# Kernel optimization log

Hardware: AMD Instinct MI355X
Metric: run time of the kernel (lower is better)

## Reference

```python
import jax, jax.numpy as jnp
import numpy as np
import math

T, P, L, C, H, NPTS = 243, 17, 4, 128, 8, 4
DH = C // H


def _ln(x, g, b):
    m = jnp.mean(x, axis=-1, keepdims=True)
    v = jnp.mean((x - m) ** 2, axis=-1, keepdims=True)
    return (x - m) * jax.lax.rsqrt(v + 1e-5) * g + b


def _bilinear(v, grid):
    # v: [B, D, Hh, Ww]; grid: [B, Q, Pt, 2] in [-1,1], (x->W, y->H),
    # align_corners=False, zero padding (matches F.grid_sample in MSDeformAttn core)
    B, D, Hh, Ww = v.shape
    x = (grid[..., 0] + 1.0) * (Ww * 0.5) - 0.5
    y = (grid[..., 1] + 1.0) * (Hh * 0.5) - 0.5
    x0 = jnp.floor(x)
    y0 = jnp.floor(y)
    x0i = x0.astype(jnp.int32)
    y0i = y0.astype(jnp.int32)
    x1i = x0i + 1
    y1i = y0i + 1
    wx1 = x - x0
    wx0 = 1.0 - wx1
    wy1 = y - y0
    wy0 = 1.0 - wy1
    vf = v.reshape(B, D, Hh * Ww)
    Q, Pt = x.shape[1], x.shape[2]

    def gather(yi, xi):
        valid = ((yi >= 0) & (yi < Hh) & (xi >= 0) & (xi < Ww)).astype(v.dtype)
        idx = jnp.clip(yi, 0, Hh - 1) * Ww + jnp.clip(xi, 0, Ww - 1)
        g = jnp.take_along_axis(vf, idx.reshape(B, 1, Q * Pt), axis=2).reshape(B, D, Q, Pt)
        return g * valid[:, None]

    return (gather(y0i, x0i) * (wy0 * wx0)[:, None]
            + gather(y0i, x1i) * (wy0 * wx1)[:, None]
            + gather(y1i, x0i) * (wy1 * wx0)[:, None]
            + gather(y1i, x1i) * (wy1 * wx1)[:, None])  # [B, D, Q, Pt]


def _forward(x, ref_points, pe_buf, learn_pos, w_off, b_off, w_attn, b_attn,
             w_val, b_val, w_out, b_out, in_w, in_b, out_w, out_b,
             fc1_w, fc1_b, fc2_w, fc2_b, g1, be1, g2, be2, g3, be3):
    b, t, p, l, c = x.shape  # l = n_levels + 1
    Lq = t * p * L
    x0 = x[..., :1, :]
    xs = x[..., 1:, :].reshape(b, Lq, c)
    # --- subforward_self: norm_1 -> PE(query) -> MSDeformAttn ---
    xn = _ln(xs, g1, be1)
    q = (xn.reshape(b, t, p, L, c) + pe_buf + learn_pos).reshape(b, Lq, c)
    off = (q @ w_off.T + b_off).reshape(b, Lq, H, L, NPTS, 2)
    aw = jax.nn.softmax((q @ w_attn.T + b_attn).reshape(b, Lq, H, L * NPTS), axis=-1)
    aw = aw.reshape(b, Lq, H, L, NPTS)
    ref = jnp.broadcast_to(ref_points[:, :, :, None, :], (b, t, p, L, 2)).reshape(b, Lq, 2)
    normalizer = jnp.array([p, t], dtype=x.dtype)  # (W, H) per level
    loc = ref[:, :, None, None, None, :] + off / normalizer  # [b,Lq,H,L,Pt,2]
    grids = 2.0 * loc - 1.0
    val = (xn @ w_val.T + b_val).reshape(b, t, p, L, H, DH)
    v_maps = val.transpose(3, 0, 4, 5, 1, 2).reshape(L, b * H, DH, t, p)
    g = grids.transpose(3, 0, 2, 1, 4, 5).reshape(L, b * H, Lq, NPTS, 2)
    sampled = jax.vmap(_bilinear)(v_maps, g)  # [L, b*H, DH, Lq, Pt]
    aw_t = aw.transpose(3, 0, 2, 1, 4).reshape(L, b * H, 1, Lq, NPTS)
    o = jnp.sum(sampled * aw_t, axis=(0, 4))  # [b*H, DH, Lq]
    o = o.reshape(b, H, DH, Lq).transpose(0, 3, 1, 2).reshape(b, Lq, c)
    xs = (o @ w_out.T + b_out) + xs
    # --- concat level-0 back, cross (self) MHA over (p*l) tokens per frame ---
    xcat = jnp.concatenate([x0, xs.reshape(b, t, p, L, c)], axis=3).reshape(b * t, p * l, c)
    xn2 = _ln(xcat, g2, be2)
    qkv = xn2 @ in_w.T + in_b
    qh, kh, vh = jnp.split(qkv, 3, axis=-1)
    S = p * l
    qh = qh.reshape(b * t, S, H, DH)
    kh = kh.reshape(b * t, S, H, DH)
    vh = vh.reshape(b * t, S, H, DH)
    att = jax.nn.softmax(jnp.einsum('bqhd,bkhd->bhqk', qh, kh) / math.sqrt(DH), axis=-1)
    ca = jnp.einsum('bhqk,bkhd->bqhd', att, vh).reshape(b * t, S, c) @ out_w.T + out_b
    xcat = ca + xcat
    xr = xcat.reshape(b, t, p, l, c)
    # --- MLP block ---
    h = _ln(xr, g3, be3)
    h = jax.nn.gelu(h @ fc1_w.T + fc1_b, approximate=False) @ fc2_w.T + fc2_b
    return h + xr


def setup_inputs() -> dict:
    key = jax.random.key(0)
    ks = jax.random.split(key, 20)
    B = 2
    s = 0.02
    x = jax.random.normal(ks[0], (B, T, P, L + 1, C), jnp.float32)
    ref_points = jax.random.uniform(ks[1], (B, T, P, 2), dtype=jnp.float32)
    # sinusoidal PE buffer
    pos = np.arange(T, dtype=np.float32)[:, None]
    div = np.exp(np.arange(0, C, 2, dtype=np.float32) * (-math.log(10000.0) / C))
    ang = pos * div  # [T, C//2]
    pe = np.zeros((1, T, P, L, C), np.float32)
    pe[..., 0::2] = np.sin(ang)[None, :, None, None, :]
    pe[..., 1::2] = np.cos(ang)[None, :, None, None, :]
    rn = lambda k, shp: s * jax.random.normal(k, shp, jnp.float32)
    return {
        'x': x, 'ref_points': ref_points,
        'pe_buf': jnp.asarray(pe),
        'learn_pos': rn(ks[2], (1, T, P, L, C)),
        'w_off': rn(ks[3], (H * L * NPTS * 2, C)), 'b_off': rn(ks[4], (H * L * NPTS * 2,)),
        'w_attn': rn(ks[5], (H * L * NPTS, C)), 'b_attn': rn(ks[6], (H * L * NPTS,)),
        'w_val': rn(ks[7], (C, C)), 'b_val': rn(ks[8], (C,)),
        'w_out': rn(ks[9], (C, C)), 'b_out': rn(ks[10], (C,)),
        'in_w': rn(ks[11], (3 * C, C)), 'in_b': rn(ks[12], (3 * C,)),
        'out_w': rn(ks[13], (C, C)), 'out_b': rn(ks[14], (C,)),
        'fc1_w': rn(ks[15], (4 * C, C)), 'fc1_b': rn(ks[16], (4 * C,)),
        'fc2_w': rn(ks[17], (C, 4 * C)), 'fc2_b': rn(ks[18], (C,)),
        'g1': jnp.ones((C,), jnp.float32), 'be1': jnp.zeros((C,), jnp.float32),
        'g2': jnp.ones((C,), jnp.float32), 'be2': jnp.zeros((C,), jnp.float32),
        'g3': jnp.ones((C,), jnp.float32), 'be3': jnp.zeros((C,), jnp.float32),
    }


def reference(x, ref_points, pe_buf, learn_pos, w_off, b_off, w_attn, b_attn,
              w_val, b_val, w_out, b_out, in_w, in_b, out_w, out_b,
              fc1_w, fc1_b, fc2_w, fc2_b, g1, be1, g2, be2, g3, be3):
    return _forward(x, ref_points, pe_buf, learn_pos, w_off, b_off, w_attn, b_attn,
                    w_val, b_val, w_out, b_out, in_w, in_b, out_w, out_b,
                    fc1_w, fc1_b, fc2_w, fc2_b, g1, be1, g2, be2, g3, be3)
```

## Files before the change

### kernel.cpp

```cpp
#include <hip/hip_runtime.h>
#include <math.h>

#define T_ 243
#define P_ 17
#define L_ 4
#define C_ 128
#define H_ 8
#define NPTS_ 4
#define DH_ 16
#define B_ 2
#define LQ (T_*P_*L_)
#define NT1 (B_*LQ)
#define LL (L_+1)
#define S_ (P_*LL)
#define NT2 (B_*T_*P_*LL)

typedef __attribute__((ext_vector_type(8))) short short8v;
typedef __attribute__((ext_vector_type(4))) short short4v;
typedef __attribute__((ext_vector_type(4))) float float4v;

__device__ __forceinline__ unsigned short f2bf(float f){
  union { float f; unsigned u; } un; un.f = f;
  unsigned r = un.u + 0x7FFF + ((un.u >> 16) & 1);
  return (unsigned short)(r >> 16);
}
__device__ __forceinline__ float bf2f(unsigned short u){
  union { unsigned u; float f; } un; un.u = ((unsigned)u) << 16; return un.f;
}
__device__ __forceinline__ void dma16(const unsigned short* g, unsigned short* l){
  __builtin_amdgcn_global_load_lds(
      (const __attribute__((address_space(1))) void*)g,
      (__attribute__((address_space(3))) void*)l, 16, 0, 0);
}

__global__ void k_wcvt(const float* __restrict__ w0, const float* __restrict__ w1,
                       const float* __restrict__ w2, const float* __restrict__ w3,
                       const float* __restrict__ w4, const float* __restrict__ w5,
                       const float* __restrict__ w6, const float* __restrict__ w7,
                       unsigned short* __restrict__ dst){
  int i = blockIdx.x*256 + threadIdx.x;
  if (i >= 278528) return;
  float v;
  if      (i < 32768)  v = w0[i];
  else if (i < 49152)  v = w1[i-32768];
  else if (i < 65536)  v = w2[i-49152];
  else if (i < 81920)  v = w3[i-65536];
  else if (i < 131072) v = w4[i-81920];
  else if (i < 147456) v = w5[i-131072];
  else if (i < 212992) v = w6[i-147456];
  else                 v = w7[i-212992];
  dst[i] = f2bf(v);
}

__global__ __launch_bounds__(256) void k_ln1_q(
    const float* __restrict__ x, const float* __restrict__ pe,
    const float* __restrict__ lpos, const float* __restrict__ g1,
    const float* __restrict__ be1, unsigned short* __restrict__ xn,
    unsigned short* __restrict__ q) {
  int w = threadIdx.x >> 6; int lane = threadIdx.x & 63;
  int i = blockIdx.x*4 + w;
  int c = lane*2;
  int b = i / LQ; int r = i % LQ;
  int t = r / (P_*L_); int rp = r % (P_*L_);
  int p = rp / L_; int lv = rp % L_;
  const float* xrow = x + (((size_t)(b*T_+t)*P_ + p)*LL + 1 + lv)*C_;
  float2 v = *(const float2*)(xrow + c);
  float s1 = v.x + v.y, s2 = v.x*v.x + v.y*v.y;
  #pragma unroll
  for (int d=1; d<64; d<<=1){ s1 += __shfl_xor(s1,d); s2 += __shfl_xor(s2,d); }
  float mean = s1*(1.0f/C_);
  float var  = s2*(1.0f/C_) - mean*mean;
  float inv = rsqrtf(var + 1e-5f);
  float2 gg = *(const float2*)(g1 + c);
  float2 bb = *(const float2*)(be1 + c);
  float xn0 = (v.x - mean)*inv*gg.x + bb.x;
  float xn1 = (v.y - mean)*inv*gg.y + bb.y;
  size_t oi = (size_t)i*C_ + c;
  *(unsigned*)(xn + oi) = (unsigned)f2bf(xn0) | ((unsigned)f2bf(xn1) << 16);
  size_t pidx = (((size_t)t*P_ + p)*L_ + lv)*C_ + c;
  float2 pv = *(const float2*)(pe + pidx);
  float2 lp = *(const float2*)(lpos + pidx);
  *(unsigned*)(q + oi) = (unsigned)f2bf(xn0 + pv.x + lp.x) | ((unsigned)f2bf(xn1 + pv.y + lp.y) << 16);
}

__global__ __launch_bounds__(256) void k_ln(
    const float* __restrict__ in, const float* __restrict__ g,
    const float* __restrict__ be, unsigned short* __restrict__ out, int M){
  int w = threadIdx.x >> 6; int lane = threadIdx.x & 63;
  int i = blockIdx.x*4 + w;
  if (i >= M) return;
  int c = lane*2;
  float2 v = *(const float2*)(in + (size_t)i*C_ + c);
  float s1 = v.x + v.y, s2 = v.x*v.x + v.y*v.y;
  #pragma unroll
  for (int d=1; d<64; d<<=1){ s1 += __shfl_xor(s1,d); s2 += __shfl_xor(s2,d); }
  float mean = s1*(1.0f/C_);
  float var  = s2*(1.0f/C_) - mean*mean;
  float inv = rsqrtf(var + 1e-5f);
  float2 gg = *(const float2*)(g + c);
  float2 bb = *(const float2*)(be + c);
  float o0 = (v.x - mean)*inv*gg.x + bb.x;
  float o1 = (v.y - mean)*inv*gg.y + bb.y;
  *(unsigned*)(out + (size_t)i*C_ + c) = (unsigned)f2bf(o0) | ((unsigned)f2bf(o1) << 16);
}

template<int K, int N, int EPI>
__global__ __launch_bounds__(256) void k_mm(
    const unsigned short* __restrict__ A, const unsigned short* __restrict__ Bw,
    const float* __restrict__ bias, const float* __restrict__ res,
    float* __restrict__ outF, unsigned short* __restrict__ outB,
    const float* __restrict__ xres, int M)
{
  constexpr int NST = K / 128;
  __shared__ unsigned short As[64*128];
  __shared__ unsigned short Bs[128*128];
  int tid = threadIdx.x;
  int lane = tid & 63;
  int w = tid >> 6;
  int lr = lane & 15, kg = lane >> 4;
  int m0 = blockIdx.x * 64;
  int n0 = blockIdx.y * 128;
  int lrow = lane >> 4;
  int lch  = lane & 15;
  float4v acc[8] = {};
  for (int st = 0; st < NST; ++st){
    int kk = st*128;
    if (st) __syncthreads();
    #pragma unroll
    for (int j = 0; j < 4; ++j){
      int rb = w*16 + j*4;
      int srcch = lch ^ ((rb + lrow) & 7);
      dma16(A + (size_t)(m0 + rb + lrow)*K + kk + srcch*8, As + rb*128);
    }
    #pragma unroll
    for (int j = 0; j < 8; ++j){
      int rb = w*32 + j*4;
      int srcch = lch ^ ((rb + lrow) & 7);
      dma16(Bw + (size_t)(n0 + rb + lrow)*K + kk + srcch*8, Bs + rb*128);
    }
    __syncthreads();
    #pragma unroll
    for (int ks = 0; ks < 4; ++ks){
      int cn = ks*4 + kg;
      int arow = w*16 + lr;
      short8v af = *(const short8v*)(As + arow*128 + ((cn ^ (arow & 7)) * 8));
      #pragma unroll
      for (int nf = 0; nf < 8; ++nf){
        int brow = nf*16 + lr;
        short8v bf = *(const short8v*)(Bs + brow*128 + ((cn ^ (brow & 7)) * 8));
        acc[nf] = __builtin_amdgcn_mfma_f32_16x16x32_bf16(af, bf, acc[nf], 0, 0, 0);
      }
    }
  }
  #pragma unroll
  for (int j = 0; j < 4; ++j){
    int gr = m0 + w*16 + kg*4 + j;
    if (gr >= M) continue;
    int b=0,t=0,p=0,lv=0;
    if (EPI == 2){
      b = gr / LQ; int r = gr % LQ;
      t = r / (P_*L_); int rp = r % (P_*L_);
      p = rp / L_; lv = rp % L_;
    }
    #pragma unroll
    for (int nf = 0; nf < 8; ++nf){
      int gc = n0 + nf*16 + lr;
      float v = acc[nf][j] + bias[gc];
      if (EPI == 0) {
        outF[(size_t)gr*N + gc] = v;
      } else if (EPI == 2) {
        size_t xi = ((((size_t)(b*T_+t)*P_ + p)*LL) + 1 + lv)*(size_t)C_ + gc;
        outF[xi] = v + xres[xi];
      } else if (EPI == 3) {
        outF[(size_t)gr*N + gc] = v + res[(size_t)gr*N + gc];
      } else if (EPI == 4) {
        float gv = 0.5f*v*(1.0f + erff(v*0.70710678118654752440f));
        outB[(size_t)gr*N + gc] = f2bf(gv);
      } else if (EPI == 5) {
        outB[(size_t)gr*N + gc] = f2bf(v);
      }
    }
  }
}

__global__ __launch_bounds__(256) void k_sample(
    const unsigned short* __restrict__ off, const unsigned short* __restrict__ awl,
    const float* __restrict__ refp, const unsigned short* __restrict__ vmap,
    unsigned short* __restrict__ o){
  int gid = blockIdx.x*256 + threadIdx.x;
  if (gid >= NT1*H_) return;
  int h = gid & 7; int i = gid >> 3;
  int b = i / LQ; int r = i % LQ;
  int t = r/(P_*L_); int rp = r%(P_*L_); int p = rp/L_;
  size_t rpi = (((size_t)b*T_+t)*P_+p)*2;
  float refx = refp[rpi + 0]*P_ - 0.5f;
  float refy = refp[rpi + 1]*T_ - 0.5f;

  float offv[32];
  {
    const short8v* op8 = (const short8v*)(off + (size_t)i*256 + h*32);
    #pragma unroll
    for (int s=0;s<4;++s){ short8v v = op8[s];
      #pragma unroll
      for (int j=0;j<8;++j) offv[s*8+j] = bf2f((unsigned short)v[j]); }
  }
  float awv[16];
  {
    const short8v* ap8 = (const short8v*)(awl + (size_t)i*128 + h*16);
    #pragma unroll
    for (int s=0;s<2;++s){ short8v v = ap8[s];
      #pragma unroll
      for (int j=0;j<8;++j) awv[s*8+j] = bf2f((unsigned short)v[j]); }
  }
  float m = awv[0];
  #pragma unroll
  for (int k=1;k<16;++k) m = fmaxf(m, awv[k]);
  float sum = 0.f;
  #pragma unroll
  for (int k=0;k<16;++k){ awv[k] = __expf(awv[k]-m); sum += awv[k]; }
  float inv = 1.f/sum;
  #pragma unroll
  for (int k=0;k<16;++k) awv[k] *= inv;

  float acc[16];
  #pragma unroll
  for (int d=0;d<16;++d) acc[d]=0.f;

  #pragma unroll
  for (int lv=0; lv<L_; ++lv){
    const unsigned short* vlv = vmap + ((size_t)b*LQ + lv)*128 + h*16;
    #pragma unroll
    for (int pt=0; pt<NPTS_; ++pt){
      float px = refx + offv[(lv*4+pt)*2+0];
      float py = refy + offv[(lv*4+pt)*2+1];
      float w  = awv[lv*4+pt];
      float fx = floorf(px), fy = floorf(py);
      int x0 = (int)fx, y0 = (int)fy;
      float wx1 = px - fx, wx0 = 1.f - wx1;
      float wy1 = py - fy, wy0 = 1.f - wy1;
      float cw[4] = {w*wy0*wx0, w*wy0*wx1, w*wy1*wx0, w*wy1*wx1};
      int ys[4] = {y0, y0, y0+1, y0+1};
      int xs[4] = {x0, x0+1, x0, x0+1};
      #pragma unroll
      for (int cidx=0; cidx<4; ++cidx){
        int yy = ys[cidx], xx = xs[cidx];
        if (yy>=0 && yy<T_ && xx>=0 && xx<P_){
          const short8v* vp = (const short8v*)(vlv + (size_t)(yy*P_ + xx)*(L_*128));
          short8v v0 = vp[0], v1 = vp[1];
          float wgt = cw[cidx];
          #pragma unroll
          for (int d=0;d<8;++d){
            acc[d]   = fmaf(wgt, bf2f((unsigned short)v0[d]), acc[d]);
            acc[8+d] = fmaf(wgt, bf2f((unsigned short)v1[d]), acc[8+d]);
          }
        }
      }
    }
  }
  short8v o0, o1;
  #pragma unroll
  for (int d=0;d<8;++d){ o0[d] = (short)f2bf(acc[d]); o1[d] = (short)f2bf(acc[8+d]); }
  short8v* op = (short8v*)(o + (size_t)i*C_ + h*DH_);
  op[0] = o0; op[1] = o1;
}

__global__ void k_copy_x0(const float* __restrict__ x, float* __restrict__ xcat){
  size_t idx = (size_t)blockIdx.x*blockDim.x + threadIdx.x;
  const size_t n = (size_t)B_*T_*P_*C_;
  if (idx < n){
    size_t c = idx % C_; size_t btp = idx / C_;
    size_t xi = (btp*LL)*C_ + c;
    xcat[xi] = x[xi];
  }
}

#define AT5_WAVE 5312
__global__ __launch_bounds__(128) void k_attn5(const unsigned short* __restrict__ qkv,
                                               unsigned short* __restrict__ ca){
  __shared__ unsigned short alds[2*AT5_WAVE];
  int w = threadIdx.x >> 6; int lane = threadIdx.x & 63;
  int bt = blockIdx.x >> 2; int hp = blockIdx.x & 3;
  int h = hp*2 + w;
  unsigned short* Kb = alds + w*AT5_WAVE;
  unsigned short* Vb = Kb + 1920;
  unsigned short* Pb = Kb + 3648;
  const unsigned short* base = qkv + (size_t)bt*85*384 + h*16;
  for (int idx = lane; idx < 192; idx += 64){
    int s = idx >> 1; int d0 = (idx & 1)*8;
    short8v kv = {}, vv = {};
    if (s < 85){
      const unsigned short* rp = base + (size_t)s*384 + d0;
      kv = *(const short8v*)(rp + 128);
      vv = *(const short8v*)(rp + 256);
    }
    *(short8v*)(Kb + s*20 + d0) = kv;
    #pragma unroll
    for (int j=0;j<8;++j) Vb[(d0+j)*108 + s] = (unsigned short)vv[j];
  }
  __syncthreads();
  int g = lane >> 4; int li = lane & 15;
  const short8v zero8 = {};
  short8v qf_cur = zero8;
  if (g < 2 && li < 85) qf_cur = *(const short8v*)(base + (size_t)li*384 + g*8);
  #pragma unroll 1
  for (int qt = 0; qt < 6; ++qt){
    short8v qf_next = zero8;
    int qn = (qt+1)*16 + li;
    if (qt < 5 && g < 2 && qn < 85)
      qf_next = *(const short8v*)(base + (size_t)qn*384 + g*8);
    float4v sc[6];
    #pragma unroll
    for (int kt = 0; kt < 6; ++kt){
      short8v kf = zero8;
      if (g < 2) kf = *(const short8v*)(Kb + (kt*16 + li)*20 + g*8);
      float4v z = {};
      sc[kt] = __builtin_amdgcn_mfma_f32_16x16x32_bf16(kf, qf_cur, z, 0, 0, 0);
    }
    float m = -1e30f;
    #pragma unroll
    for (int kt = 0; kt < 6; ++kt)
      #pragma unroll
      for (int j = 0; j < 4; ++j){
        float v = sc[kt][j]*0.25f;
        if (kt == 5 && (g*4 + j) >= 5) v = -1e30f;
        sc[kt][j] = v;
        m = fmaxf(m, v);
      }
    m = fmaxf(m, __shfl_xor(m, 16));
    m = fmaxf(m, __shfl_xor(m, 32));
    float sum = 0.f;
    #pragma unroll
    for (int kt = 0; kt < 6; ++kt){
      short4v pf;
      #pragma unroll
      for (int j = 0; j < 4; ++j){
        float e = __expf(sc[kt][j] - m);
        sum += e;
        pf[j] = (short)f2bf(e);
      }
      *(short4v*)(Pb + li*104 + kt*16 + g*4) = pf;
    }
    sum += __shfl_xor(sum, 16);
    sum += __shfl_xor(sum, 32);
    float inv = 1.f/sum;
    float4v oacc = {};
    #pragma unroll
    for (int kt32 = 0; kt32 < 3; ++kt32){
      short8v vf  = *(const short8v*)(Vb + li*108 + kt32*32 + g*8);
      short8v pf8 = *(const short8v*)(Pb + li*104 + kt32*32 + g*8);
      oacc = __builtin_amdgcn_mfma_f32_16x16x32_bf16(vf, pf8, oacc, 0, 0, 0);
    }
    int q = qt*16 + li;
    if (q < 85){
      short4v ov;
      #pragma unroll
      for (int j=0;j<4;++j) ov[j] = (short)f2bf(oacc[j]*inv);
      *(short4v*)(ca + ((size_t)bt*85 + q)*128 + h*16 + g*4) = ov;
    }
    qf_cur = qf_next;
  }
}

extern "C" void kernel_launch(void* const* d_in, const int* in_sizes, int n_in,
                              void* d_out, int out_size, void* d_ws, size_t ws_size,
                              hipStream_t stream) {
  (void)in_sizes; (void)n_in; (void)out_size; (void)ws_size;
  const float* x      = (const float*)d_in[0];
  const float* refp   = (const float*)d_in[1];
  const float* pe     = (const float*)d_in[2];
  const float* lpos   = (const float*)d_in[3];
  const float* w_off  = (const float*)d_in[4];
  const float* b_off  = (const float*)d_in[5];
  const float* w_attn = (const float*)d_in[6];
  const float* b_attn = (const float*)d_in[7];
  const float* w_val  = (const float*)d_in[8];
  const float* b_val  = (const float*)d_in[9];
  const float* w_out  = (const float*)d_in[10];
  const float* b_out  = (const float*)d_in[11];
  const float* in_w   = (const float*)d_in[12];
  const float* in_b   = (const float*)d_in[13];
  const float* out_w  = (const float*)d_in[14];
  const float* out_b  = (const float*)d_in[15];
  const float* fc1_w  = (const float*)d_in[16];
  const float* fc1_b  = (const float*)d_in[17];
  const float* fc2_w  = (const float*)d_in[18];
  const float* fc2_b  = (const float*)d_in[19];
  const float* g1     = (const float*)d_in[20];
  const float* be1    = (const float*)d_in[21];
  const float* g2     = (const float*)d_in[22];
  const float* be2    = (const float*)d_in[23];
  const float* g3     = (const float*)d_in[24];
  const float* be3    = (const float*)d_in[25];
  float* out = (float*)d_out;
  char* wsb = (char*)d_ws;

  unsigned short* xn_b  = (unsigned short*)(wsb + 0);
  unsigned short* q_b   = (unsigned short*)(wsb + 8460288);
  unsigned short* off_b = (unsigned short*)(wsb + 16920576);
  unsigned short* aw_b  = (unsigned short*)(wsb + 33841152);
  unsigned short* vm_b  = (unsigned short*)(wsb + 42301440);
  unsigned short* o_b   = (unsigned short*)(wsb + 50761728);
  float*          xcatB = (float*)(wsb + 59222016);
  unsigned short* xn2_b = (unsigned short*)(wsb + 80372736);
  unsigned short* qkv_b = (unsigned short*)(wsb + 90948096);
  unsigned short* wb    = (unsigned short*)(wsb + 122674176);
  unsigned short* ca_b  = (unsigned short*)(wsb + 0);
  unsigned short* ln3_b = (unsigned short*)(wsb + 80372736);
  unsigned short* hid_b = (unsigned short*)(wsb + 16920576);

  unsigned short* wb_off  = wb + 0;
  unsigned short* wb_attn = wb + 32768;
  unsigned short* wb_val  = wb + 49152;
  unsigned short* wb_wout = wb + 65536;
  unsigned short* wb_in   = wb + 81920;
  unsigned short* wb_outw = wb + 131072;
  unsigned short* wb_fc1  = wb + 147456;
  unsigned short* wb_fc2  = wb + 212992;

  const int GM1 = (NT1 + 63)/64;
  const int GM2 = (NT2 + 63)/64;

  hipLaunchKernelGGL(k_wcvt, dim3((278528+255)/256), dim3(256), 0, stream,
                     w_off, w_attn, w_val, w_out, in_w, out_w, fc1_w, fc2_w, wb);
  hipLaunchKernelGGL(k_ln1_q, dim3(NT1/4), dim3(256), 0, stream, x, pe, lpos, g1, be1, xn_b, q_b);
  hipLaunchKernelGGL((k_mm<128,256,5>), dim3(GM1,2), dim3(256), 0, stream,
                     q_b, wb_off, b_off, nullptr, nullptr, off_b, nullptr, NT1);
  hipLaunchKernelGGL((k_mm<128,128,5>), dim3(GM1,1), dim3(256), 0, stream,
                     q_b, wb_attn, b_attn, nullptr, nullptr, aw_b, nullptr, NT1);
  hipLaunchKernelGGL((k_mm<128,128,5>), dim3(GM1,1), dim3(256), 0, stream,
                     xn_b, wb_val, b_val, nullptr, nullptr, vm_b, nullptr, NT1);
  hipLaunchKernelGGL(k_sample, dim3((NT1*H_+255)/256), dim3(256), 0, stream,
                     off_b, aw_b, refp, vm_b, o_b);
  hipLaunchKernelGGL((k_mm<128,128,2>), dim3(GM1,1), dim3(256), 0, stream,
                     o_b, wb_wout, b_out, nullptr, xcatB, nullptr, x, NT1);
  hipLaunchKernelGGL(k_copy_x0, dim3(((size_t)B_*T_*P_*C_+255)/256), dim3(256), 0, stream, x, xcatB);
  hipLaunchKernelGGL(k_ln, dim3((NT2+3)/4), dim3(256), 0, stream, xcatB, g2, be2, xn2_b, NT2);
  hipLaunchKernelGGL((k_mm<128,384,5>), dim3(GM2,3), dim3(256), 0, stream,
                     xn2_b, wb_in, in_b, nullptr, nullptr, qkv_b, nullptr, NT2);
  hipLaunchKernelGGL(k_attn5, dim3(B_*T_*4), dim3(128), 0, stream, qkv_b, ca_b);
  hipLaunchKernelGGL((k_mm<128,128,3>), dim3(GM2,1), dim3(256), 0, stream,
                     ca_b, wb_outw, out_b, xcatB, xcatB, nullptr, nullptr, NT2);
  hipLaunchKernelGGL(k_ln, dim3((NT2+3)/4), dim3(256), 0, stream, xcatB, g3, be3, ln3_b, NT2);
  hipLaunchKernelGGL((k_mm<128,512,4>), dim3(GM2,4), dim3(256), 0, stream,
                     ln3_b, wb_fc1, fc1_b, nullptr, nullptr, hid_b, nullptr, NT2);
  hipLaunchKernelGGL((k_mm<512,128,3>), dim3(GM2,1), dim3(256), 0, stream,
                     hid_b, wb_fc2, fc2_b, xcatB, out, nullptr, nullptr, NT2);
}
```

Baseline: 221.7 us.

## Fuse LayerNorms into GEMM epilogues and merge three projection GEMMs

Merges the offset, attention-weight and value projections into one launch over a 4-wide grid, with blockIdx.y choosing the input and the output buffer. LayerNorm 2 and LayerNorm 3 move into the residual epilogues of the preceding output-projection GEMMs, computing row statistics with 16-lane shuffles since each block holds a full 128-column row. The x0 copy is fused with LayerNorm for the x0 rows. The goal is fewer kernel launches and fewer full-tensor re-reads, at the cost of heavier epilogues and scattered bf16 stores.

```diff
diff --git a/kernel.cpp b/kernel.cpp
--- a/kernel.cpp
+++ b/kernel.cpp
@@ -83,25 +83,29 @@
   *(unsigned*)(q + oi) = (unsigned)f2bf(xn0 + pv.x + lp.x) | ((unsigned)f2bf(xn1 + pv.y + lp.y) << 16);
 }
 
-__global__ __launch_bounds__(256) void k_ln(
-    const float* __restrict__ in, const float* __restrict__ g,
-    const float* __restrict__ be, unsigned short* __restrict__ out, int M){
+__global__ __launch_bounds__(256) void k_x0ln(
+    const float* __restrict__ x, const float* __restrict__ g2,
+    const float* __restrict__ be2, float* __restrict__ xcat,
+    unsigned short* __restrict__ xn2){
   int w = threadIdx.x >> 6; int lane = threadIdx.x & 63;
   int i = blockIdx.x*4 + w;
-  if (i >= M) return;
+  if (i >= B_*T_*P_) return;
   int c = lane*2;
-  float2 v = *(const float2*)(in + (size_t)i*C_ + c);
+  size_t xrow = (size_t)i*LL;
+  const float* xr = x + xrow*C_;
+  float2 v = *(const float2*)(xr + c);
   float s1 = v.x + v.y, s2 = v.x*v.x + v.y*v.y;
   #pragma unroll
   for (int d=1; d<64; d<<=1){ s1 += __shfl_xor(s1,d); s2 += __shfl_xor(s2,d); }
   float mean = s1*(1.0f/C_);
   float var  = s2*(1.0f/C_) - mean*mean;
   float inv = rsqrtf(var + 1e-5f);
-  float2 gg = *(const float2*)(g + c);
-  float2 bb = *(const float2*)(be + c);
+  float2 gg = *(const float2*)(g2 + c);
+  float2 bb = *(const float2*)(be2 + c);
+  *(float2*)(xcat + xrow*C_ + c) = v;
   float o0 = (v.x - mean)*inv*gg.x + bb.x;
   float o1 = (v.y - mean)*inv*gg.y + bb.y;
-  *(unsigned*)(out + (size_t)i*C_ + c) = (unsigned)f2bf(o0) | ((unsigned)f2bf(o1) << 16);
+  *(unsigned*)(xn2 + xrow*C_ + c) = (unsigned)f2bf(o0) | ((unsigned)f2bf(o1) << 16);
 }
 
 template<int K, int N, int EPI>
@@ -109,7 +113,8 @@
     const unsigned short* __restrict__ A, const unsigned short* __restrict__ Bw,
     const float* __restrict__ bias, const float* __restrict__ res,
     float* __restrict__ outF, unsigned short* __restrict__ outB,
-    const float* __restrict__ xres, int M)
+    const float* __restrict__ xres, const float* __restrict__ lng,
+    const float* __restrict__ lnbe, int M)
 {
   constexpr int NST = K / 128;
   __shared__ unsigned short As[64*128];
@@ -156,29 +161,115 @@
   for (int j = 0; j < 4; ++j){
     int gr = m0 + w*16 + kg*4 + j;
     if (gr >= M) continue;
-    int b=0,t=0,p=0,lv=0;
-    if (EPI == 2){
-      b = gr / LQ; int r = gr % LQ;
-      t = r / (P_*L_); int rp = r % (P_*L_);
-      p = rp / L_; lv = rp % L_;
-    }
+    if (EPI == 3 || EPI == 4 || EPI == 5){
+      #pragma unroll
+      for (int nf = 0; nf < 8; ++nf){
+        int gc = n0 + nf*16 + lr;
+        float v = acc[nf][j] + bias[gc];
+        if (EPI == 3) {
+          outF[(size_t)gr*N + gc] = v + res[(size_t)gr*N + gc];
+        } else if (EPI == 4) {
+          float gv = 0.5f*v*(1.0f + erff(v*0.70710678118654752440f));
+          outB[(size_t)gr*N + gc] = f2bf(gv);
+        } else {
+          outB[(size_t)gr*N + gc] = f2bf(v);
+        }
+      }
+    } else {
+      size_t xrow;
+      if (EPI == 6){
+        int b = gr / LQ; int r = gr % LQ;
+        int t = r / (P_*L_); int rp = r % (P_*L_);
+        int p = rp / L_; int lv = rp % L_;
+        xrow = (((size_t)(b*T_+t)*P_ + p)*LL) + 1 + lv;
+      } else {
+        xrow = (size_t)gr;
+      }
+      float vals[8];
+      float s = 0.f, sq = 0.f;
+      #pragma unroll
+      for (int nf = 0; nf < 8; ++nf){
+        int gc = n0 + nf*16 + lr;
+        float v = acc[nf][j] + bias[gc];
+        if (EPI == 6) v += xres[xrow*C_ + gc];
+        else          v += res[xrow*C_ + gc];
+        vals[nf] = v; s += v; sq += v*v;
+      }
+      #pragma unroll
+      for (int d = 1; d < 16; d <<= 1){ s += __shfl_xor(s, d); sq += __shfl_xor(sq, d); }
+      float mean = s*(1.0f/128.f);
+      float varr = sq*(1.0f/128.f) - mean*mean;
+      float linv = rsqrtf(varr + 1e-5f);
+      #pragma unroll
+      for (int nf = 0; nf < 8; ++nf){
+        int gc = n0 + nf*16 + lr;
+        outF[xrow*C_ + gc] = vals[nf];
+        float ln = (vals[nf] - mean)*linv*lng[gc] + lnbe[gc];
+        outB[xrow*C_ + gc] = f2bf(ln);
+      }
+    }
+  }
+}
+
+__global__ __launch_bounds__(256) void k_mm3(
+    const unsigned short* __restrict__ Aq, const unsigned short* __restrict__ Axn,
+    const unsigned short* __restrict__ Bw,
+    const float* __restrict__ b_off, const float* __restrict__ b_attn,
+    const float* __restrict__ b_val,
+    unsigned short* __restrict__ off_b, unsigned short* __restrict__ aw_b,
+    unsigned short* __restrict__ vm_b, int M)
+{
+  __shared__ unsigned short As[64*128];
+  __shared__ unsigned short Bs[128*128];
+  int tid = threadIdx.x;
+  int lane = tid & 63;
+  int w = tid >> 6;
+  int lr = lane & 15, kg = lane >> 4;
+  int m0 = blockIdx.x * 64;
+  int y  = blockIdx.y;
+  int n0 = y * 128;
+  const unsigned short* A = (y == 3) ? Axn : Aq;
+  int lrow = lane >> 4;
+  int lch  = lane & 15;
+  float4v acc[8] = {};
+  #pragma unroll
+  for (int j = 0; j < 4; ++j){
+    int rb = w*16 + j*4;
+    int srcch = lch ^ ((rb + lrow) & 7);
+    dma16(A + (size_t)(m0 + rb + lrow)*128 + srcch*8, As + rb*128);
+  }
+  #pragma unroll
+  for (int j = 0; j < 8; ++j){
+    int rb = w*32 + j*4;
+    int srcch = lch ^ ((rb + lrow) & 7);
+    dma16(Bw + (size_t)(n0 + rb + lrow)*128 + srcch*8, Bs + rb*128);
+  }
+  __syncthreads();
+  #pragma unroll
+  for (int ks = 0; ks < 4; ++ks){
+    int cn = ks*4 + kg;
+    int arow = w*16 + lr;
+    short8v af = *(const short8v*)(As + arow*128 + ((cn ^ (arow & 7)) * 8));
+    #pragma unroll
+    for (int nf = 0; nf < 8; ++nf){
+      int brow = nf*16 + lr;
+      short8v bf = *(const short8v*)(Bs + brow*128 + ((cn ^ (brow & 7)) * 8));
+      acc[nf] = __builtin_amdgcn_mfma_f32_16x16x32_bf16(af, bf, acc[nf], 0, 0, 0);
+    }
+  }
+  const float* bias = (y < 2) ? b_off : (y == 2 ? b_attn - 256 : b_val - 384);
+  #pragma unroll
+  for (int j = 0; j < 4; ++j){
+    int gr = m0 + w*16 + kg*4 + j;
+    if (gr >= M) continue;
     #pragma unroll
     for (int nf = 0; nf < 8; ++nf){
       int gc = n0 + nf*16 + lr;
       float v = acc[nf][j] + bias[gc];
-      if (EPI == 0) {
-        outF[(size_t)gr*N + gc] = v;
-      } else if (EPI == 2) {
-        size_t xi = ((((size_t)(b*T_+t)*P_ + p)*LL) + 1 + lv)*(size_t)C_ + gc;
-        outF[xi] = v + xres[xi];
-      } else if (EPI == 3) {
-        outF[(size_t)gr*N + gc] = v + res[(size_t)gr*N + gc];
-      } else if (EPI == 4) {
-        float gv = 0.5f*v*(1.0f + erff(v*0.70710678118654752440f));
-        outB[(size_t)gr*N + gc] = f2bf(gv);
-      } else if (EPI == 5) {
-        outB[(size_t)gr*N + gc] = f2bf(v);
-      }
+      unsigned short bv = f2bf(v);
+      if (y < 2)      off_b[(size_t)gr*256 + gc]       = bv;
+      else if (y==2)  aw_b [(size_t)gr*128 + gc - 256] = bv;
+      else            vm_b [(size_t)gr*128 + gc - 384] = bv;
     }
   }
 }
@@ -262,16 +353,6 @@
   for (int d=0;d<8;++d){ o0[d] = (short)f2bf(acc[d]); o1[d] = (short)f2bf(acc[8+d]); }
   short8v* op = (short8v*)(o + (size_t)i*C_ + h*DH_);
   op[0] = o0; op[1] = o1;
-}
-
-__global__ void k_copy_x0(const float* __restrict__ x, float* __restrict__ xcat){
-  size_t idx = (size_t)blockIdx.x*blockDim.x + threadIdx.x;
-  const size_t n = (size_t)B_*T_*P_*C_;
-  if (idx < n){
-    size_t c = idx % C_; size_t btp = idx / C_;
-    size_t xi = (btp*LL)*C_ + c;
-    xcat[xi] = x[xi];
-  }
 }
 
 #define AT5_WAVE 5312
@@ -409,8 +490,6 @@
   unsigned short* hid_b = (unsigned short*)(wsb + 16920576);
 
   unsigned short* wb_off  = wb + 0;
-  unsigned short* wb_attn = wb + 32768;
-  unsigned short* wb_val  = wb + 49152;
   unsigned short* wb_wout = wb + 65536;
   unsigned short* wb_in   = wb + 81920;
   unsigned short* wb_outw = wb + 131072;
@@ -423,26 +502,20 @@
   hipLaunchKernelGGL(k_wcvt, dim3((278528+255)/256), dim3(256), 0, stream,
                      w_off, w_attn, w_val, w_out, in_w, out_w, fc1_w, fc2_w, wb);
   hipLaunchKernelGGL(k_ln1_q, dim3(NT1/4), dim3(256), 0, stream, x, pe, lpos, g1, be1, xn_b, q_b);
-  hipLaunchKernelGGL((k_mm<128,256,5>), dim3(GM1,2), dim3(256), 0, stream,
-                     q_b, wb_off, b_off, nullptr, nullptr, off_b, nullptr, NT1);
-  hipLaunchKernelGGL((k_mm<128,128,5>), dim3(GM1,1), dim3(256), 0, stream,
-                     q_b, wb_attn, b_attn, nullptr, nullptr, aw_b, nullptr, NT1);
-  hipLaunchKernelGGL((k_mm<128,128,5>), dim3(GM1,1), dim3(256), 0, stream,
-                     xn_b, wb_val, b_val, nullptr, nullptr, vm_b, nullptr, NT1);
+  hipLaunchKernelGGL(k_mm3, dim3(GM1,4), dim3(256), 0, stream,
+                     q_b, xn_b, wb_off, b_off, b_attn, b_val, off_b, aw_b, vm_b, NT1);
   hipLaunchKernelGGL(k_sample, dim3((NT1*H_+255)/256), dim3(256), 0, stream,
                      off_b, aw_b, refp, vm_b, o_b);
-  hipLaunchKernelGGL((k_mm<128,128,2>), dim3(GM1,1), dim3(256), 0, stream,
-                     o_b, wb_wout, b_out, nullptr, xcatB, nullptr, x, NT1);
-  hipLaunchKernelGGL(k_copy_x0, dim3(((size_t)B_*T_*P_*C_+255)/256), dim3(256), 0, stream, x, xcatB);
-  hipLaunchKernelGGL(k_ln, dim3((NT2+3)/4), dim3(256), 0, stream, xcatB, g2, be2, xn2_b, NT2);
+  hipLaunchKernelGGL((k_mm<128,128,6>), dim3(GM1,1), dim3(256), 0, stream,
+                     o_b, wb_wout, b_out, nullptr, xcatB, xn2_b, x, g2, be2, NT1);
+  hipLaunchKernelGGL(k_x0ln, dim3((B_*T_*P_+3)/4), dim3(256), 0, stream, x, g2, be2, xcatB, xn2_b);
   hipLaunchKernelGGL((k_mm<128,384,5>), dim3(GM2,3), dim3(256), 0, stream,
-                     xn2_b, wb_in, in_b, nullptr, nullptr, qkv_b, nullptr, NT2);
+                     xn2_b, wb_in, in_b, nullptr, nullptr, qkv_b, nullptr, nullptr, nullptr, NT2);
   hipLaunchKernelGGL(k_attn5, dim3(B_*T_*4), dim3(128), 0, stream, qkv_b, ca_b);
-  hipLaunchKernelGGL((k_mm<128,128,3>), dim3(GM2,1), dim3(256), 0, stream,
-                     ca_b, wb_outw, out_b, xcatB, xcatB, nullptr, nullptr, NT2);
-  hipLaunchKernelGGL(k_ln, dim3((NT2+3)/4), dim3(256), 0, stream, xcatB, g3, be3, ln3_b, NT2);
+  hipLaunchKernelGGL((k_mm<128,128,7>), dim3(GM2,1), dim3(256), 0, stream,
+                     ca_b, wb_outw, out_b, xcatB, xcatB, ln3_b, nullptr, g3, be3, NT2);
   hipLaunchKernelGGL((k_mm<128,512,4>), dim3(GM2,4), dim3(256), 0, stream,
-                     ln3_b, wb_fc1, fc1_b, nullptr, nullptr, hid_b, nullptr, NT2);
+                     ln3_b, wb_fc1, fc1_b, nullptr, nullptr, hid_b, nullptr, nullptr, nullptr, NT2);
   hipLaunchKernelGGL((k_mm<512,128,3>), dim3(GM2,1), dim3(256), 0, stream,
-                     hid_b, wb_fc2, fc2_b, xcatB, out, nullptr, nullptr, NT2);
-}
+                     hid_b, wb_fc2, fc2_b, xcatB, out, nullptr, nullptr, nullptr, nullptr, NT2);
+}
```

Result: faster. 212.5 us (-4.2%).
